# Kernel optimization log

Measured on AMD Instinct MI355X. Metric: run time of the kernel, lower is better.

Reference implementation:

```python
import jax, jax.numpy as jnp
import numpy as np

B, C, T = 32, 512, 1024
SIG_LO, SIG_HI = 1.0, 10.0   # sigma_range
THR, BETA = 0.5, 0.95        # snn.Leaky(beta=0.95, threshold=thr)
KSIZE = 13


def setup_inputs() -> dict:
    key = jax.random.key(0)
    inp = jax.random.normal(key, (B, 1, C, T), dtype=jnp.float32)
    # nn.Parameter initialized to sigma_range.mean() = 5.5
    w = jnp.float32((SIG_LO + SIG_HI) / 2.0)
    return {"inp": inp, "w": w}


def _gaussian_kernel(sigma):
    # matches gaussian_kernel(size=13): linspace(-6, 6, 13), normalized
    r = jnp.linspace(-(KSIZE // 2), KSIZE // 2, KSIZE).astype(jnp.float32)
    k = jnp.exp(-0.5 * (r / sigma) ** 2)
    return k / k.sum()


def _atan_spike(u):
    # snntorch default ATan surrogate (alpha=2): fwd heaviside, bwd 1/(1+(pi*u)^2)
    soft = jnp.arctan(jnp.pi * u) / jnp.pi
    hard = (u > 0).astype(u.dtype)
    return soft + jax.lax.stop_gradient(hard - soft)


def reference(inp, w):
    x = inp[:, 0]  # (B, C, T)
    # w_eff = sigma_range.mean() + clamp(w, 1, 10); identical for every sample,
    # so the per-sample/per-timestep kernels of the original are all equal.
    sigma = (SIG_LO + SIG_HI) / 2.0 + jnp.clip(w, SIG_LO, SIG_HI)
    k = _gaussian_kernel(sigma)  # (13,)
    # 13-tap Gaussian smoothing along the channel axis, all timesteps at once
    x_mean = jax.lax.conv_general_dilated(
        x[:, None],                    # (B,1,C,T)
        k[None, None, :, None],        # (1,1,13,1)
        window_strides=(1, 1),
        padding=((KSIZE // 2, KSIZE // 2), (0, 0)),
        dimension_numbers=("NCHW", "OIHW", "NCHW"),
    )[:, 0]                            # (B,C,T)
    drive = jnp.transpose(x - x_mean, (2, 0, 1))  # (T,B,C)

    def step(mem, xt):
        # snntorch Leaky, reset_mechanism='subtract'; reset is detached
        reset = jax.lax.stop_gradient((mem > THR).astype(mem.dtype))
        mem = BETA * mem + xt - reset * THR
        spk = _atan_spike(mem - THR)
        return mem, spk

    mem0 = jnp.zeros((B, C), dtype=jnp.float32)
    _, spks = jax.lax.scan(step, mem0, drive)  # (T,B,C)
    return jnp.transpose(spks, (1, 2, 0))[:, None]  # (B,1,C,T)
```

## Files before the change

kernel.cpp:

```cpp
#include <hip/hip_runtime.h>
#include <math.h>

constexpr int Bn = 32;
constexpr int Cn = 512;
constexpr int Tn = 1024;
constexpr int KS = 13;

constexpr int CB   = 64;
constexpr int TT   = 64;
constexpr int NCH  = Tn / TT;
constexpr int DSTR = TT + 1;
constexpr int NB   = 4;
constexpr int NL   = 34;


#define SCAN16(DV, TB)                                                   \
  _Pragma("unroll")                                                      \
  for (int j = 0; j < 16; ++j) {                                         \
    const float rthr = (mem > 0.5f) ? 0.5f : 0.0f;   \
    float a_  = __fmul_rn(0.95f, mem);                                   \
    float s2_ = __fadd_rn(a_, DV[j]);                                    \
    mem = __fsub_rn(s2_, rthr);                                          \
    const unsigned int bit = (mem > 0.5f) ? 1u : 0u;                     \
    if ((TB) + j < 32) lo |= bit << ((TB) + j);                          \
    else               hi |= bit << ((TB) + j - 32);                     \
  }

__global__ __launch_bounds__(320, 1)
void snn_fused(const float* __restrict__ x, const float* __restrict__ wp,
               float* __restrict__ out) {
  __shared__ float D[NB][CB][DSTR];
  __shared__ unsigned long long Sb[NCH][CB];
  __shared__ unsigned int prod[NB];
  __shared__ unsigned int scanProg;

  const int tid = threadIdx.x;
  const int b   = blockIdx.y;
  const int c0  = blockIdx.x * CB;
  const long xbase = (long)b * Cn * Tn;

  if (tid < NB) prod[tid] = 0u;
  if (tid == NB) scanProg = 0u;

  float kw[KS];
  {
    float w  = wp[0];
    float wc = fminf(fmaxf(w, 1.0f), 10.0f);
    float sigma = __fadd_rn(5.5f, wc);
    float e[KS];
#pragma unroll
    for (int i = 0; i < KS; ++i) {
      float q = __fdiv_rn((float)(i - 6), sigma);
      float t = __fmul_rn(-0.5f, __fmul_rn(q, q));
      e[i] = (float)exp((double)t);
    }
    float s = __fadd_rn(
        __fadd_rn(__fadd_rn(e[0], e[1]), __fadd_rn(e[2], e[3])),
        __fadd_rn(__fadd_rn(e[4], e[5]), __fadd_rn(e[6], e[7])));
    s = __fadd_rn(s, e[8]);  s = __fadd_rn(s, e[9]);  s = __fadd_rn(s, e[10]);
    s = __fadd_rn(s, e[11]); s = __fadd_rn(s, e[12]);
#pragma unroll
    for (int i = 0; i < KS; ++i) kw[i] = __fdiv_rn(e[i], s);
  }

  __syncthreads();

  if (tid < 64) {
    const int c = tid;
    float mem = 0.0f;
    for (int k = 0; k < NCH; ++k) {
      const int slot = k & (NB - 1);
      const unsigned need = 3u * ((unsigned)(k / NB) + 1u);
      while (__hip_atomic_load(&prod[slot], __ATOMIC_ACQUIRE,
                               __HIP_MEMORY_SCOPE_WORKGROUP) < need) {}
      const float* Dc = &D[slot][c][0];
      unsigned int lo = 0u, hi = 0u;
      float dvA[16], dvB[16];
#pragma unroll
      for (int j = 0; j < 16; ++j) dvA[j] = Dc[j];
#pragma unroll
      for (int j = 0; j < 16; ++j) dvB[j] = Dc[16 + j];
      SCAN16(dvA, 0)
#pragma unroll
      for (int j = 0; j < 16; ++j) dvA[j] = Dc[32 + j];
      SCAN16(dvB, 16)
#pragma unroll
      for (int j = 0; j < 16; ++j) dvB[j] = Dc[48 + j];
      SCAN16(dvA, 32)
      SCAN16(dvB, 48)
      Sb[k][c] = ((unsigned long long)hi << 32) | (unsigned long long)lo;
      if (tid == 0)
        __hip_atomic_fetch_add(&scanProg, 1u, __ATOMIC_RELEASE,
                               __HIP_MEMORY_SCOPE_WORKGROUP);
    }
  } else if (tid < 256) {
    const int ctid = tid - 64;
    const int col  = ctid & 63;
    const int segS = (ctid >> 6) * 21;
    const int cin0 = c0 + segS - 6;

    float xp[NL], xn[NL];

    auto load_chunk = [&](int m, float* dst) {
#pragma unroll
      for (int j = 0; j < NL; ++j) {
        const int gc = cin0 + j;
        float v = 0.0f;
        if (gc >= 0 && gc < Cn)
          v = x[xbase + (long)gc * Tn + m * TT + col];
        dst[j] = v;
      }
    };
    auto conv_chunk = [&](const float* xs, int p) {
#pragma unroll
      for (int r = 0; r < 22; ++r) {
        float acc = __fmul_rn(kw[0], xs[r]);
#pragma unroll
        for (int i = 1; i < KS; ++i)
          acc = __fadd_rn(acc, __fmul_rn(kw[i], xs[r + i]));
        D[p][segS + r][col] = __fsub_rn(xs[r + 6], acc);
      }
    };

    load_chunk(0, xp);
    for (int k = 0; k < NCH; ++k) {
      if (k + 1 < NCH) load_chunk(k + 1, xn);
      if (k >= NB) {
        const unsigned need = (unsigned)(k - NB + 1);
        while (__hip_atomic_load(&scanProg, __ATOMIC_ACQUIRE,
                                 __HIP_MEMORY_SCOPE_WORKGROUP) < need) {}
      }
      conv_chunk(xp, k & (NB - 1));
      if (col == 0)
        __hip_atomic_fetch_add(&prod[k & (NB - 1)], 1u, __ATOMIC_RELEASE,
                               __HIP_MEMORY_SCOPE_WORKGROUP);
      if (k + 1 < NCH) {
#pragma unroll
        for (int j = 0; j < NL; ++j) xp[j] = xn[j];
      }
    }
  } else {
    const int col = tid & 63;
    for (int k = 0; k < NCH; ++k) {
      while (__hip_atomic_load(&scanProg, __ATOMIC_ACQUIRE,
                               __HIP_MEMORY_SCOPE_WORKGROUP)
             < (unsigned)(k + 1)) {}
      const int t0p = k * TT;
#pragma unroll 8
      for (int r = 0; r < CB; ++r) {
        const unsigned long long wb = Sb[k][r];
        const float v = ((wb >> col) & 1ull) ? 1.0f : 0.0f;
        out[xbase + (long)(c0 + r) * Tn + t0p + col] = v;
      }
    }
  }
}

extern "C" void kernel_launch(void* const* d_in, const int* in_sizes, int n_in,
                              void* d_out, int out_size, void* d_ws, size_t ws_size,
                              hipStream_t stream) {
  const float* x  = (const float*)d_in[0];
  const float* w  = (const float*)d_in[1];
  float* out      = (float*)d_out;
  dim3 grid(Cn / CB, Bn, 1);
  snn_fused<<<grid, 320, 0, stream>>>(x, w, out);
}
```

Measured before the change: 132.3 us.

## Add fourth conv wave and triple-buffer input loads two chunks ahead

Raises the number of convolution warps from three to four, so each handles 16 channels with a 28-row halo instead of 22 with a 34-row halo, and the block grows to 384 threads. Input chunk loads now use three rotating register buffers and prefetch two chunks ahead, which removes the register copy between buffers. The producer signal switches to a relaxed atomic preceded by an explicit s_waitcnt lgkmcnt(0) so the LDS writes are complete before the count is published. The cost is more threads and registers per block, and correctness depends on that manual wait giving the needed ordering.

```diff
diff --git a/kernel.cpp b/kernel.cpp
--- a/kernel.cpp
+++ b/kernel.cpp
@@ -11,7 +11,9 @@
 constexpr int NCH  = Tn / TT;
 constexpr int DSTR = TT + 1;
 constexpr int NB   = 4;
-constexpr int NL   = 34;
+constexpr int NCW  = 4;
+constexpr int SEG  = CB / NCW;
+constexpr int NL   = SEG + KS - 1;
 
 
 #define SCAN16(DV, TB)                                                   \
@@ -26,7 +28,7 @@
     else               hi |= bit << ((TB) + j - 32);                     \
   }
 
-__global__ __launch_bounds__(320, 1)
+__global__ __launch_bounds__(384, 1)
 void snn_fused(const float* __restrict__ x, const float* __restrict__ wp,
                float* __restrict__ out) {
   __shared__ float D[NB][CB][DSTR];
@@ -70,7 +72,7 @@
     float mem = 0.0f;
     for (int k = 0; k < NCH; ++k) {
       const int slot = k & (NB - 1);
-      const unsigned need = 3u * ((unsigned)(k / NB) + 1u);
+      const unsigned need = (unsigned)NCW * ((unsigned)(k >> 2) + 1u);
       while (__hip_atomic_load(&prod[slot], __ATOMIC_ACQUIRE,
                                __HIP_MEMORY_SCOPE_WORKGROUP) < need) {}
       const float* Dc = &D[slot][c][0];
@@ -93,13 +95,13 @@
         __hip_atomic_fetch_add(&scanProg, 1u, __ATOMIC_RELEASE,
                                __HIP_MEMORY_SCOPE_WORKGROUP);
     }
-  } else if (tid < 256) {
+  } else if (tid < 64 + 64 * NCW) {
     const int ctid = tid - 64;
     const int col  = ctid & 63;
-    const int segS = (ctid >> 6) * 21;
+    const int segS = (ctid >> 6) * SEG;
     const int cin0 = c0 + segS - 6;
 
-    float xp[NL], xn[NL];
+    float xA[NL], xB[NL], xC[NL];
 
     auto load_chunk = [&](int m, float* dst) {
 #pragma unroll
@@ -113,7 +115,7 @@
     };
     auto conv_chunk = [&](const float* xs, int p) {
 #pragma unroll
-      for (int r = 0; r < 22; ++r) {
+      for (int r = 0; r < SEG; ++r) {
         float acc = __fmul_rn(kw[0], xs[r]);
 #pragma unroll
         for (int i = 1; i < KS; ++i)
@@ -122,23 +124,31 @@
       }
     };
 
-    load_chunk(0, xp);
-    for (int k = 0; k < NCH; ++k) {
-      if (k + 1 < NCH) load_chunk(k + 1, xn);
-      if (k >= NB) {
-        const unsigned need = (unsigned)(k - NB + 1);
-        while (__hip_atomic_load(&scanProg, __ATOMIC_ACQUIRE,
-                                 __HIP_MEMORY_SCOPE_WORKGROUP) < need) {}
-      }
-      conv_chunk(xp, k & (NB - 1));
-      if (col == 0)
-        __hip_atomic_fetch_add(&prod[k & (NB - 1)], 1u, __ATOMIC_RELEASE,
-                               __HIP_MEMORY_SCOPE_WORKGROUP);
-      if (k + 1 < NCH) {
-#pragma unroll
-        for (int j = 0; j < NL; ++j) xp[j] = xn[j];
-      }
+#define STEP(K, BC, BL)                                                  \
+    do {                                                                 \
+      if ((K) + 2 < NCH) load_chunk((K) + 2, BL);                        \
+      if ((K) >= NB) {                                                   \
+        const unsigned need_ = (unsigned)((K) - NB + 1);                 \
+        while (__hip_atomic_load(&scanProg, __ATOMIC_ACQUIRE,            \
+                                 __HIP_MEMORY_SCOPE_WORKGROUP) < need_) {} \
+      }                                                                  \
+      conv_chunk(BC, (K) & (NB - 1));                                    \
+      __asm__ __volatile__("s_waitcnt lgkmcnt(0)" ::: "memory");         \
+      if (col == 0)                                                      \
+        __hip_atomic_fetch_add(&prod[(K) & (NB - 1)], 1u,                \
+                               __ATOMIC_RELAXED,                         \
+                               __HIP_MEMORY_SCOPE_WORKGROUP);            \
+    } while (0)
+
+    load_chunk(0, xA);
+    load_chunk(1, xB);
+    for (int kb = 0; kb < NCH - 1; kb += 3) {
+      STEP(kb + 0, xA, xC);
+      STEP(kb + 1, xB, xA);
+      STEP(kb + 2, xC, xB);
     }
+    STEP(NCH - 1, xA, xC);
+#undef STEP
   } else {
     const int col = tid & 63;
     for (int k = 0; k < NCH; ++k) {
@@ -163,5 +173,5 @@
   const float* w  = (const float*)d_in[1];
   float* out      = (float*)d_out;
   dim3 grid(Cn / CB, Bn, 1);
-  snn_fused<<<grid, 320, 0, stream>>>(x, w, out);
+  snn_fused<<<grid, 384, 0, stream>>>(x, w, out);
 }
```

Result: faster. 126.8 us (-4.1%).
